# Optimization experiments

Hardware: AMD Instinct MI355X
Metric: run time of the kernel (lower is better)

The kernel has to match this reference:

```python
import jax, jax.numpy as jnp
import numpy as np

N = 4096       # voc_size
D = 256        # emb_dim
NEG = -9e15    # pyGAT mask value
ALPHA = 0.2    # LeakyReLU slope


def _row_normalize(a):
    rs = a.sum(axis=1, keepdims=True)
    inv = jnp.where(rs > 0, 1.0 / rs, 0.0)
    return a * inv


def setup_inputs() -> dict:
    key = jax.random.key(0)
    ks = jax.random.split(key, 10)
    # sparse-ish symmetric adjacency, then self-loops + row-normalize (GraphAT.normalize)
    raw = (jax.random.uniform(ks[0], (N, N)) < 0.01).astype(jnp.float32)
    raw = jnp.maximum(raw, raw.T)
    adj = _row_normalize(raw + jnp.eye(N, dtype=jnp.float32))
    x = jax.random.normal(ks[1], (N, N), dtype=jnp.float32) * 0.05
    def w(k, i, o):
        return jax.random.normal(k, (i, o), dtype=jnp.float32) * (1.0 / np.sqrt(i))
    return {
        "x": x, "adj": adj,
        "W11": w(ks[2], N, D), "a11": jax.random.normal(ks[3], (2 * D, 1), jnp.float32) * 0.1,
        "W12": w(ks[4], D, D), "a12": jax.random.normal(ks[5], (2 * D, 1), jnp.float32) * 0.1,
        "W21": w(ks[6], D, D), "a21": jax.random.normal(ks[7], (2 * D, 1), jnp.float32) * 0.1,
        "W22": w(ks[8], D, D), "a22": jax.random.normal(ks[9], (2 * D, 1), jnp.float32) * 0.1,
    }


def _gat_layer(h, adj, W, a):
    # Wh: [N, d_out]
    Wh = h @ W
    d_out = W.shape[1]
    f_src = Wh @ a[:d_out]          # [N, 1]
    f_dst = Wh @ a[d_out:]          # [N, 1]
    e = jax.nn.leaky_relu(f_src + f_dst.T, ALPHA)   # [N, N]
    e = jnp.where(adj > 0, e, NEG)
    attn = jax.nn.softmax(e, axis=1)
    return attn @ Wh                # [N, d_out]


def _gat(h, adj, Wa, aa, Wb, ab):
    # pyGAT GAT: multi-head (1 head) + ELU, then output attention layer + ELU
    h = jax.nn.elu(_gat_layer(h, adj, Wa, aa))
    return jax.nn.elu(_gat_layer(h, adj, Wb, ab))


def reference(x, adj, W11, a11, W12, a12, W21, a21, W22, a22):
    h = _gat(x, adj, W11, a11, W12, a12)
    h = jax.nn.relu(h)              # dropout(p=0.3) is identity in eval mode
    return _gat(h, adj, W21, a21, W22, a22)
```

## Files before the change

### kernel.cpp

```cpp
#include <hip/hip_runtime.h>
#include <hip/hip_bf16.h>
#include <cstdint>
#include <cstddef>

#define NV 4096
#define DE 256
#define MAXNNZ 192

typedef __attribute__((ext_vector_type(8))) short bf16x8;
typedef __attribute__((ext_vector_type(4))) float f32x4;

__device__ __forceinline__ unsigned short f2bf(float f) {
    unsigned int u = __float_as_uint(f);
    u += 0x7fff + ((u >> 16) & 1);
    return (unsigned short)(u >> 16);
}
__device__ __forceinline__ float bf2f(unsigned short h) {
    return __uint_as_float(((unsigned int)h) << 16);
}

__global__ __launch_bounds__(256) void build_csr(const float* __restrict__ adj,
                                                 int* __restrict__ cols,
                                                 int* __restrict__ nnz)
{
    int wave = threadIdx.x >> 6;
    int lane = threadIdx.x & 63;
    int row  = blockIdx.x * 4 + wave;
    const float* arow = adj + (size_t)row * NV;
    int* crow = cols + (size_t)row * MAXNNZ;
    int base = 0;
    for (int c0 = 0; c0 < NV; c0 += 64) {
        float v = arow[c0 + lane];
        bool pred = v > 0.0f;
        unsigned long long m = __ballot(pred);
        int idx = base + __popcll(m & ((1ull << lane) - 1ull));
        if (pred && idx < MAXNNZ) crow[idx] = c0 + lane;
        base += __popcll(m);
    }
    if (lane == 0) nnz[row] = base < MAXNNZ ? base : MAXNNZ;
}

__global__ __launch_bounds__(256) void transp_split(const float* __restrict__ W,
                                                    unsigned short* __restrict__ bh,
                                                    unsigned short* __restrict__ bl,
                                                    int K)
{
    __shared__ float tile[32][33];
    const int k0 = blockIdx.x * 32, n0 = blockIdx.y * 32;
    const int t = threadIdx.x;
    {
        int r = t >> 3, cq = t & 7;
        float4 v = *(const float4*)&W[(size_t)(k0 + r) * DE + n0 + cq * 4];
        tile[r][cq * 4 + 0] = v.x;
        tile[r][cq * 4 + 1] = v.y;
        tile[r][cq * 4 + 2] = v.z;
        tile[r][cq * 4 + 3] = v.w;
    }
    __syncthreads();
    {
        int nl = t >> 3, kq = t & 7;
        ushort4 hv, lv;
        float x0 = tile[kq * 4 + 0][nl];
        float x1 = tile[kq * 4 + 1][nl];
        float x2 = tile[kq * 4 + 2][nl];
        float x3 = tile[kq * 4 + 3][nl];
        hv.x = f2bf(x0); lv.x = f2bf(x0 - bf2f(hv.x));
        hv.y = f2bf(x1); lv.y = f2bf(x1 - bf2f(hv.y));
        hv.z = f2bf(x2); lv.z = f2bf(x2 - bf2f(hv.z));
        hv.w = f2bf(x3); lv.w = f2bf(x3 - bf2f(hv.w));
        size_t o = (size_t)(n0 + nl) * K + k0 + kq * 4;
        *(ushort4*)&bh[o] = hv;
        *(ushort4*)&bl[o] = lv;
    }
}

#define BM 64
#define BN 64
#define BK 32

__global__ __launch_bounds__(256) void gemm_split(const float* __restrict__ A,
                                                  const unsigned short* __restrict__ Bh,
                                                  const unsigned short* __restrict__ Bl,
                                                  float* __restrict__ C,
                                                  int K, int Kchunk)
{
    __shared__ __align__(16) unsigned short sA[64 * 64];
    __shared__ __align__(16) unsigned short sB[64 * 64];

    const int t    = threadIdx.x;
    const int lane = t & 63;
    const int wid  = t >> 6;
    const int wr   = wid >> 1;
    const int wc   = wid & 1;
    const int bn   = blockIdx.x * BN;
    const int bm   = blockIdx.y * BM;
    const int kz   = blockIdx.z;
    const int kbeg = kz * Kchunk;
    const int nsteps = Kchunk / BK;

    const int ar = t >> 2;
    const int as = t & 3;
    const int br = t >> 2;
    const int bq = t & 3;

    const float*          Ap  = A  + (size_t)(bm + ar) * K + kbeg + as * 8;
    const unsigned short* Bhp = Bh + (size_t)(bn + br) * K + kbeg + bq * 8;
    const unsigned short* Blp = Bl + (size_t)(bn + br) * K + kbeg + bq * 8;

    const int aw_h = ar * 64 + (((as)      ^ (ar & 7)) << 3);
    const int aw_l = ar * 64 + (((as | 4)  ^ (ar & 7)) << 3);
    const int bw_h = br * 64 + (((bq)      ^ (br & 7)) << 3);
    const int bw_l = br * 64 + (((bq | 4)  ^ (br & 7)) << 3);

    const int fr = lane & 15, fsub = lane >> 4;
    const int arow0 = wr * 32 + fr;
    const int arow1 = arow0 + 16;
    const int ard0h = arow0 * 64 + (((fsub)     ^ (arow0 & 7)) << 3);
    const int ard0l = arow0 * 64 + (((fsub | 4) ^ (arow0 & 7)) << 3);
    const int ard1h = arow1 * 64 + (((fsub)     ^ (arow1 & 7)) << 3);
    const int ard1l = arow1 * 64 + (((fsub | 4) ^ (arow1 & 7)) << 3);
    const int brow0 = wc * 32 + fr;
    const int brow1 = brow0 + 16;
    const int brd0h = brow0 * 64 + (((fsub)     ^ (brow0 & 7)) << 3);
    const int brd0l = brow0 * 64 + (((fsub | 4) ^ (brow0 & 7)) << 3);
    const int brd1h = brow1 * 64 + (((fsub)     ^ (brow1 & 7)) << 3);
    const int brd1l = brow1 * 64 + (((fsub | 4) ^ (brow1 & 7)) << 3);

    float4 a0 = *(const float4*)(Ap);
    float4 a1 = *(const float4*)(Ap + 4);
    bf16x8 g_bh = *(const bf16x8*)(Bhp);
    bf16x8 g_bl = *(const bf16x8*)(Blp);

    f32x4 acc[2][2];
#pragma unroll
    for (int i = 0; i < 2; ++i)
#pragma unroll
        for (int j = 0; j < 2; ++j) acc[i][j] = (f32x4){0.f, 0.f, 0.f, 0.f};

    for (int s = 0; s < nsteps; ++s) {
        __syncthreads();
        {
            float xs0 = a0.x, xs1 = a0.y, xs2 = a0.z, xs3 = a0.w;
            float xs4 = a1.x, xs5 = a1.y, xs6 = a1.z, xs7 = a1.w;
            bf16x8 hv, lv;
            unsigned short h;
            h = f2bf(xs0); hv[0] = (short)h; lv[0] = (short)f2bf(xs0 - bf2f(h));
            h = f2bf(xs1); hv[1] = (short)h; lv[1] = (short)f2bf(xs1 - bf2f(h));
            h = f2bf(xs2); hv[2] = (short)h; lv[2] = (short)f2bf(xs2 - bf2f(h));
            h = f2bf(xs3); hv[3] = (short)h; lv[3] = (short)f2bf(xs3 - bf2f(h));
            h = f2bf(xs4); hv[4] = (short)h; lv[4] = (short)f2bf(xs4 - bf2f(h));
            h = f2bf(xs5); hv[5] = (short)h; lv[5] = (short)f2bf(xs5 - bf2f(h));
            h = f2bf(xs6); hv[6] = (short)h; lv[6] = (short)f2bf(xs6 - bf2f(h));
            h = f2bf(xs7); hv[7] = (short)h; lv[7] = (short)f2bf(xs7 - bf2f(h));
            *(bf16x8*)&sA[aw_h] = hv;
            *(bf16x8*)&sA[aw_l] = lv;
        }
        *(bf16x8*)&sB[bw_h] = g_bh;
        *(bf16x8*)&sB[bw_l] = g_bl;
        __syncthreads();

        if (s + 1 < nsteps) {
            Ap += BK; Bhp += BK; Blp += BK;
            a0 = *(const float4*)(Ap);
            a1 = *(const float4*)(Ap + 4);
            g_bh = *(const bf16x8*)(Bhp);
            g_bl = *(const bf16x8*)(Blp);
        }

        bf16x8 ah0 = *(const bf16x8*)&sA[ard0h];
        bf16x8 al0 = *(const bf16x8*)&sA[ard0l];
        bf16x8 ah1 = *(const bf16x8*)&sA[ard1h];
        bf16x8 al1 = *(const bf16x8*)&sA[ard1l];
        bf16x8 bh0 = *(const bf16x8*)&sB[brd0h];
        bf16x8 bl0 = *(const bf16x8*)&sB[brd0l];
        bf16x8 bh1 = *(const bf16x8*)&sB[brd1h];
        bf16x8 bl1 = *(const bf16x8*)&sB[brd1l];

        acc[0][0] = __builtin_amdgcn_mfma_f32_16x16x32_bf16(ah0, bh0, acc[0][0], 0, 0, 0);
        acc[0][0] = __builtin_amdgcn_mfma_f32_16x16x32_bf16(ah0, bl0, acc[0][0], 0, 0, 0);
        acc[0][0] = __builtin_amdgcn_mfma_f32_16x16x32_bf16(al0, bh0, acc[0][0], 0, 0, 0);
        acc[0][1] = __builtin_amdgcn_mfma_f32_16x16x32_bf16(ah0, bh1, acc[0][1], 0, 0, 0);
        acc[0][1] = __builtin_amdgcn_mfma_f32_16x16x32_bf16(ah0, bl1, acc[0][1], 0, 0, 0);
        acc[0][1] = __builtin_amdgcn_mfma_f32_16x16x32_bf16(al0, bh1, acc[0][1], 0, 0, 0);
        acc[1][0] = __builtin_amdgcn_mfma_f32_16x16x32_bf16(ah1, bh0, acc[1][0], 0, 0, 0);
        acc[1][0] = __builtin_amdgcn_mfma_f32_16x16x32_bf16(ah1, bl0, acc[1][0], 0, 0, 0);
        acc[1][0] = __builtin_amdgcn_mfma_f32_16x16x32_bf16(al1, bh0, acc[1][0], 0, 0, 0);
        acc[1][1] = __builtin_amdgcn_mfma_f32_16x16x32_bf16(ah1, bh1, acc[1][1], 0, 0, 0);
        acc[1][1] = __builtin_amdgcn_mfma_f32_16x16x32_bf16(ah1, bl1, acc[1][1], 0, 0, 0);
        acc[1][1] = __builtin_amdgcn_mfma_f32_16x16x32_bf16(al1, bh1, acc[1][1], 0, 0, 0);
    }

    float* Cb = C + (size_t)kz * NV * DE;
#pragma unroll
    for (int mi = 0; mi < 2; ++mi) {
#pragma unroll
        for (int ni = 0; ni < 2; ++ni) {
            int row = bm + wr * 32 + mi * 16 + (fsub << 2);
            int col = bn + wc * 32 + ni * 16 + fr;
#pragma unroll
            for (int i = 0; i < 4; ++i)
                Cb[(size_t)(row + i) * DE + col] = acc[mi][ni][i];
        }
    }
}

__global__ __launch_bounds__(256) void reduce_fsd(const float* __restrict__ Cp,
                                                  const float* __restrict__ a,
                                                  float* __restrict__ Wh,
                                                  float* __restrict__ fs,
                                                  float* __restrict__ fd,
                                                  int S)
{
    int wid = threadIdx.x >> 6, lane = threadIdx.x & 63;
    int row = blockIdx.x * 4 + wid;
    size_t idx = (size_t)row * DE + lane * 4;
    float4 w = *(const float4*)&Cp[idx];
    for (int s = 1; s < S; ++s) {
        float4 p = *(const float4*)&Cp[(size_t)s * NV * DE + idx];
        w.x += p.x; w.y += p.y; w.z += p.z; w.w += p.w;
    }
    *(float4*)&Wh[idx] = w;
    float4 at = *(const float4*)&a[lane * 4];
    float4 ab = *(const float4*)&a[DE + lane * 4];
    float s = w.x * at.x + w.y * at.y + w.z * at.z + w.w * at.w;
    float d = w.x * ab.x + w.y * ab.y + w.z * ab.z + w.w * ab.w;
#pragma unroll
    for (int off = 32; off; off >>= 1) {
        s += __shfl_down(s, off);
        d += __shfl_down(d, off);
    }
    if (lane == 0) { fs[row] = s; fd[row] = d; }
}

template <int ACT>
__global__ __launch_bounds__(256) void attn_spmm(const float* __restrict__ Wh,
                                                 const float* __restrict__ fs,
                                                 const float* __restrict__ fd,
                                                 const int* __restrict__ cols,
                                                 const int* __restrict__ nnzArr,
                                                 float* __restrict__ out)
{
    __shared__ float p[MAXNNZ];
    __shared__ int   ci[MAXNNZ];
    __shared__ float red[4];
    __shared__ float part[4][DE];

    const int row = blockIdx.x;
    const int t   = threadIdx.x;
    const int lane = t & 63;
    const int wv   = t >> 6;
    const int n   = nnzArr[row];
    const int* rc = cols + (size_t)row * MAXNNZ;
    const float fsi = fs[row];

    float lm = -1e30f;
    for (int j = t; j < n; j += 256) {
        int c = rc[j];
        ci[j] = c;
        float e = fsi + fd[c];
        e = (e >= 0.0f) ? e : 0.2f * e;
        p[j] = e;
        lm = fmaxf(lm, e);
    }
#pragma unroll
    for (int off = 32; off; off >>= 1) lm = fmaxf(lm, __shfl_down(lm, off));
    if (lane == 0) red[wv] = lm;
    __syncthreads();
    const float m = fmaxf(fmaxf(red[0], red[1]), fmaxf(red[2], red[3]));
    __syncthreads();

    float ls = 0.0f;
    for (int j = t; j < n; j += 256) {
        float pe = expf(p[j] - m);
        p[j] = pe;
        ls += pe;
    }
#pragma unroll
    for (int off = 32; off; off >>= 1) ls += __shfl_down(ls, off);
    if (lane == 0) red[wv] = ls;
    __syncthreads();
    const float invZ = 1.0f / (red[0] + red[1] + red[2] + red[3]);

    const int d4 = lane * 4;
    f32x4 acc = (f32x4){0.f, 0.f, 0.f, 0.f};
    int j = wv;
    for (; j + 4 < n; j += 8) {
        float pj0 = p[j];     int c0 = ci[j];
        float pj1 = p[j + 4]; int c1 = ci[j + 4];
        float4 w0 = *(const float4*)&Wh[(size_t)c0 * DE + d4];
        float4 w1 = *(const float4*)&Wh[(size_t)c1 * DE + d4];
        acc.x = fmaf(pj0, w0.x, acc.x);
        acc.y = fmaf(pj0, w0.y, acc.y);
        acc.z = fmaf(pj0, w0.z, acc.z);
        acc.w = fmaf(pj0, w0.w, acc.w);
        acc.x = fmaf(pj1, w1.x, acc.x);
        acc.y = fmaf(pj1, w1.y, acc.y);
        acc.z = fmaf(pj1, w1.z, acc.z);
        acc.w = fmaf(pj1, w1.w, acc.w);
    }
    for (; j < n; j += 4) {
        float pj = p[j]; int c = ci[j];
        float4 w0 = *(const float4*)&Wh[(size_t)c * DE + d4];
        acc.x = fmaf(pj, w0.x, acc.x);
        acc.y = fmaf(pj, w0.y, acc.y);
        acc.z = fmaf(pj, w0.z, acc.z);
        acc.w = fmaf(pj, w0.w, acc.w);
    }
    *(f32x4*)&part[wv][d4] = acc;
    __syncthreads();

    float v = (part[0][t] + part[1][t]) + (part[2][t] + part[3][t]);
    v *= invZ;
    float r;
    if (ACT == 0) r = (v > 0.0f) ? v : expm1f(v);
    else          r = (v > 0.0f) ? v : 0.0f;
    out[(size_t)row * DE + t] = r;
}

extern "C" void kernel_launch(void* const* d_in, const int* in_sizes, int n_in,
                              void* d_out, int out_size, void* d_ws, size_t ws_size,
                              hipStream_t stream)
{
    const float* x   = (const float*)d_in[0];
    const float* adj = (const float*)d_in[1];
    const float* W11 = (const float*)d_in[2];
    const float* a11 = (const float*)d_in[3];
    const float* W12 = (const float*)d_in[4];
    const float* a12 = (const float*)d_in[5];
    const float* W21 = (const float*)d_in[6];
    const float* a21 = (const float*)d_in[7];
    const float* W22 = (const float*)d_in[8];
    const float* a22 = (const float*)d_in[9];
    float* out = (float*)d_out;

    char* ws = (char*)d_ws;
    size_t off = 0;
    int*   cols = (int*)(ws + off);            off += (size_t)NV * MAXNNZ * 4;
    int*   nnz  = (int*)(ws + off);            off += 16 * 1024;
    float* fs   = (float*)(ws + off);          off += 16 * 1024;
    float* fd   = (float*)(ws + off);          off += 16 * 1024;
    float* Wh   = (float*)(ws + off);          off += (size_t)NV * DE * 4;
    float* hA   = (float*)(ws + off);          off += (size_t)NV * DE * 4;
    unsigned short* BtH = (unsigned short*)(ws + off); off += (size_t)DE * NV * 2;
    unsigned short* BtL = (unsigned short*)(ws + off); off += (size_t)DE * NV * 2;
    float* Cpart = (float*)(ws + off);

    build_csr<<<NV / 4, 256, 0, stream>>>(adj, cols, nnz);

    transp_split<<<dim3(NV / 32, DE / 32), 256, 0, stream>>>(W11, BtH, BtL, NV);
    gemm_split<<<dim3(DE / BN, NV / BM, 4), 256, 0, stream>>>(x, BtH, BtL, Cpart, NV, NV / 4);
    reduce_fsd<<<NV / 4, 256, 0, stream>>>(Cpart, a11, Wh, fs, fd, 4);
    attn_spmm<0><<<NV, 256, 0, stream>>>(Wh, fs, fd, cols, nnz, hA);

    transp_split<<<dim3(DE / 32, DE / 32), 256, 0, stream>>>(W12, BtH, BtL, DE);
    gemm_split<<<dim3(DE / BN, NV / BM, 2), 256, 0, stream>>>(hA, BtH, BtL, Cpart, DE, DE / 2);
    reduce_fsd<<<NV / 4, 256, 0, stream>>>(Cpart, a12, Wh, fs, fd, 2);
    attn_spmm<1><<<NV, 256, 0, stream>>>(Wh, fs, fd, cols, nnz, hA);

    transp_split<<<dim3(DE / 32, DE / 32), 256, 0, stream>>>(W21, BtH, BtL, DE);
    gemm_split<<<dim3(DE / BN, NV / BM, 2), 256, 0, stream>>>(hA, BtH, BtL, Cpart, DE, DE / 2);
    reduce_fsd<<<NV / 4, 256, 0, stream>>>(Cpart, a21, Wh, fs, fd, 2);
    attn_spmm<0><<<NV, 256, 0, stream>>>(Wh, fs, fd, cols, nnz, hA);

    transp_split<<<dim3(DE / 32, DE / 32), 256, 0, stream>>>(W22, BtH, BtL, DE);
    gemm_split<<<dim3(DE / BN, NV / BM, 2), 256, 0, stream>>>(hA, BtH, BtL, Cpart, DE, DE / 2);
    reduce_fsd<<<NV / 4, 256, 0, stream>>>(Cpart, a22, Wh, fs, fd, 2);
    attn_spmm<0><<<NV, 256, 0, stream>>>(Wh, fs, fd, cols, nnz, out);
}
```

Measured before the change: 194.1 us.

## Enlarge GEMM tiles, add XCD-aware block remap, pre-split activations, vectorize CSR build

Replaces the 64x64 split-bf16 GEMM with a 128x128-tile version using a 4x4 MFMA accumulator grid per wave and an XCD-aware block index remap. The split-K factor is doubled. The attention SpMM kernel now writes its output pre-split into bf16 hi/lo arrays, so later GEMMs skip the per-tile fp32-to-bf16 split. The CSR builder reads the adjacency matrix with float4 loads. The larger tiles cut global re-reads of A and B, at the cost of more registers, fewer blocks and more split-K partials to reduce.

```diff
diff --git a/kernel.cpp b/kernel.cpp
--- a/kernel.cpp
+++ b/kernel.cpp
@@ -29,13 +29,17 @@
     const float* arow = adj + (size_t)row * NV;
     int* crow = cols + (size_t)row * MAXNNZ;
     int base = 0;
-    for (int c0 = 0; c0 < NV; c0 += 64) {
-        float v = arow[c0 + lane];
-        bool pred = v > 0.0f;
-        unsigned long long m = __ballot(pred);
-        int idx = base + __popcll(m & ((1ull << lane) - 1ull));
-        if (pred && idx < MAXNNZ) crow[idx] = c0 + lane;
-        base += __popcll(m);
+    for (int c0 = 0; c0 < NV; c0 += 256) {
+        float4 v = *(const float4*)&arow[c0 + lane * 4];
+        float vv[4] = {v.x, v.y, v.z, v.w};
+#pragma unroll
+        for (int e = 0; e < 4; ++e) {
+            bool pred = vv[e] > 0.0f;
+            unsigned long long m = __ballot(pred);
+            int idx = base + __popcll(m & ((1ull << lane) - 1ull));
+            if (pred && idx < MAXNNZ) crow[idx] = c0 + lane * 4 + e;
+            base += __popcll(m);
+        }
     }
     if (lane == 0) nnz[row] = base < MAXNNZ ? base : MAXNNZ;
 }
@@ -74,129 +78,139 @@
     }
 }
 
-#define BM 64
-#define BN 64
-#define BK 32
-
-__global__ __launch_bounds__(256) void gemm_split(const float* __restrict__ A,
+template <bool PRESPLIT>
+__global__ __launch_bounds__(256, 2) void gemm_bt(const float* __restrict__ Af,
+                                                  const unsigned short* __restrict__ Ah,
+                                                  const unsigned short* __restrict__ Al,
                                                   const unsigned short* __restrict__ Bh,
                                                   const unsigned short* __restrict__ Bl,
                                                   float* __restrict__ C,
                                                   int K, int Kchunk)
 {
-    __shared__ __align__(16) unsigned short sA[64 * 64];
-    __shared__ __align__(16) unsigned short sB[64 * 64];
-
-    const int t    = threadIdx.x;
-    const int lane = t & 63;
-    const int wid  = t >> 6;
-    const int wr   = wid >> 1;
-    const int wc   = wid & 1;
-    const int bn   = blockIdx.x * BN;
-    const int bm   = blockIdx.y * BM;
-    const int kz   = blockIdx.z;
+    __shared__ __align__(16) unsigned short sA[128 * 64];
+    __shared__ __align__(16) unsigned short sB[128 * 64];
+
+    const int t = threadIdx.x, lane = t & 63, wid = t >> 6;
+    const int wr = wid >> 1, wc = wid & 1;
+    const int KZ = K / Kchunk;
+
+    const int nwg = gridDim.x, orig = blockIdx.x;
+    const int q = nwg >> 3, r = nwg & 7;
+    const int xcd = orig & 7, jj = orig >> 3;
+    const int wgid = (xcd < r ? xcd * (q + 1) : r * (q + 1) + (xcd - r) * q) + jj;
+    const int row_t = wgid & 31;
+    const int kz    = (wgid >> 5) % KZ;
+    const int colt  = wgid / (32 * KZ);
+    const int bm = row_t * 128, bn = colt * 128;
     const int kbeg = kz * Kchunk;
-    const int nsteps = Kchunk / BK;
-
-    const int ar = t >> 2;
-    const int as = t & 3;
-    const int br = t >> 2;
-    const int bq = t & 3;
-
-    const float*          Ap  = A  + (size_t)(bm + ar) * K + kbeg + as * 8;
-    const unsigned short* Bhp = Bh + (size_t)(bn + br) * K + kbeg + bq * 8;
-    const unsigned short* Blp = Bl + (size_t)(bn + br) * K + kbeg + bq * 8;
-
-    const int aw_h = ar * 64 + (((as)      ^ (ar & 7)) << 3);
-    const int aw_l = ar * 64 + (((as | 4)  ^ (ar & 7)) << 3);
-    const int bw_h = br * 64 + (((bq)      ^ (br & 7)) << 3);
-    const int bw_l = br * 64 + (((bq | 4)  ^ (br & 7)) << 3);
+    const int nsteps = Kchunk / 32;
+
+    const int srow = t >> 1, shalf = t & 1;
+    const float*          Afp = Af ? (Af + (size_t)(bm + srow) * K + kbeg + shalf * 16) : nullptr;
+    const unsigned short* Ahp = Ah ? (Ah + (size_t)(bm + srow) * K + kbeg + shalf * 16) : nullptr;
+    const unsigned short* Alp = Al ? (Al + (size_t)(bm + srow) * K + kbeg + shalf * 16) : nullptr;
+    const unsigned short* Bhp = Bh + (size_t)(bn + srow) * K + kbeg + shalf * 16;
+    const unsigned short* Blp = Bl + (size_t)(bn + srow) * K + kbeg + shalf * 16;
+
+    const int c0 = shalf * 2;
+    const int wa0 = srow * 64 + (((c0)           ^ (srow & 7)) << 3);
+    const int wa1 = srow * 64 + (((c0 + 1)       ^ (srow & 7)) << 3);
+    const int wa2 = srow * 64 + (((c0 | 4)       ^ (srow & 7)) << 3);
+    const int wa3 = srow * 64 + ((((c0 + 1) | 4) ^ (srow & 7)) << 3);
 
     const int fr = lane & 15, fsub = lane >> 4;
-    const int arow0 = wr * 32 + fr;
-    const int arow1 = arow0 + 16;
-    const int ard0h = arow0 * 64 + (((fsub)     ^ (arow0 & 7)) << 3);
-    const int ard0l = arow0 * 64 + (((fsub | 4) ^ (arow0 & 7)) << 3);
-    const int ard1h = arow1 * 64 + (((fsub)     ^ (arow1 & 7)) << 3);
-    const int ard1l = arow1 * 64 + (((fsub | 4) ^ (arow1 & 7)) << 3);
-    const int brow0 = wc * 32 + fr;
-    const int brow1 = brow0 + 16;
-    const int brd0h = brow0 * 64 + (((fsub)     ^ (brow0 & 7)) << 3);
-    const int brd0l = brow0 * 64 + (((fsub | 4) ^ (brow0 & 7)) << 3);
-    const int brd1h = brow1 * 64 + (((fsub)     ^ (brow1 & 7)) << 3);
-    const int brd1l = brow1 * 64 + (((fsub | 4) ^ (brow1 & 7)) << 3);
-
-    float4 a0 = *(const float4*)(Ap);
-    float4 a1 = *(const float4*)(Ap + 4);
-    bf16x8 g_bh = *(const bf16x8*)(Bhp);
-    bf16x8 g_bl = *(const bf16x8*)(Blp);
-
-    f32x4 acc[2][2];
-#pragma unroll
-    for (int i = 0; i < 2; ++i)
-#pragma unroll
-        for (int j = 0; j < 2; ++j) acc[i][j] = (f32x4){0.f, 0.f, 0.f, 0.f};
+
+    bf16x8 gah0, gah1, gal0, gal1, gbh0, gbh1, gbl0, gbl1;
+
+#define LOAD_TILE()                                                          \
+    do {                                                                     \
+        if (PRESPLIT) {                                                      \
+            gah0 = *(const bf16x8*)(Ahp);                                    \
+            gah1 = *(const bf16x8*)(Ahp + 8);                                \
+            gal0 = *(const bf16x8*)(Alp);                                    \
+            gal1 = *(const bf16x8*)(Alp + 8);                                \
+        } else {                                                             \
+            float4 f0 = *(const float4*)(Afp);                               \
+            float4 f1 = *(const float4*)(Afp + 4);                           \
+            float4 f2 = *(const float4*)(Afp + 8);                           \
+            float4 f3 = *(const float4*)(Afp + 12);                          \
+            float xs[16] = {f0.x, f0.y, f0.z, f0.w, f1.x, f1.y, f1.z, f1.w,  \
+                            f2.x, f2.y, f2.z, f2.w, f3.x, f3.y, f3.z, f3.w}; \
+            _Pragma("unroll") for (int e = 0; e < 8; ++e) {                  \
+                unsigned short h = f2bf(xs[e]);                              \
+                gah0[e] = (short)h;                                          \
+                gal0[e] = (short)f2bf(xs[e] - bf2f(h));                      \
+            }                                                                \
+            _Pragma("unroll") for (int e = 0; e < 8; ++e) {                  \
+                unsigned short h = f2bf(xs[8 + e]);                          \
+                gah1[e] = (short)h;                                          \
+                gal1[e] = (short)f2bf(xs[8 + e] - bf2f(h));                  \
+            }                                                                \
+        }                                                                    \
+        gbh0 = *(const bf16x8*)(Bhp);                                        \
+        gbh1 = *(const bf16x8*)(Bhp + 8);                                    \
+        gbl0 = *(const bf16x8*)(Blp);                                        \
+        gbl1 = *(const bf16x8*)(Blp + 8);                                    \
+    } while (0)
+
+    LOAD_TILE();
+
+    f32x4 acc[4][4];
+#pragma unroll
+    for (int i = 0; i < 4; ++i)
+#pragma unroll
+        for (int j2 = 0; j2 < 4; ++j2) acc[i][j2] = (f32x4){0.f, 0.f, 0.f, 0.f};
 
     for (int s = 0; s < nsteps; ++s) {
         __syncthreads();
-        {
-            float xs0 = a0.x, xs1 = a0.y, xs2 = a0.z, xs3 = a0.w;
-            float xs4 = a1.x, xs5 = a1.y, xs6 = a1.z, xs7 = a1.w;
-            bf16x8 hv, lv;
-            unsigned short h;
-            h = f2bf(xs0); hv[0] = (short)h; lv[0] = (short)f2bf(xs0 - bf2f(h));
-            h = f2bf(xs1); hv[1] = (short)h; lv[1] = (short)f2bf(xs1 - bf2f(h));
-            h = f2bf(xs2); hv[2] = (short)h; lv[2] = (short)f2bf(xs2 - bf2f(h));
-            h = f2bf(xs3); hv[3] = (short)h; lv[3] = (short)f2bf(xs3 - bf2f(h));
-            h = f2bf(xs4); hv[4] = (short)h; lv[4] = (short)f2bf(xs4 - bf2f(h));
-            h = f2bf(xs5); hv[5] = (short)h; lv[5] = (short)f2bf(xs5 - bf2f(h));
-            h = f2bf(xs6); hv[6] = (short)h; lv[6] = (short)f2bf(xs6 - bf2f(h));
-            h = f2bf(xs7); hv[7] = (short)h; lv[7] = (short)f2bf(xs7 - bf2f(h));
-            *(bf16x8*)&sA[aw_h] = hv;
-            *(bf16x8*)&sA[aw_l] = lv;
-        }
-        *(bf16x8*)&sB[bw_h] = g_bh;
-        *(bf16x8*)&sB[bw_l] = g_bl;
+        *(bf16x8*)&sA[wa0] = gah0;
+        *(bf16x8*)&sA[wa1] = gah1;
+        *(bf16x8*)&sA[wa2] = gal0;
+        *(bf16x8*)&sA[wa3] = gal1;
+        *(bf16x8*)&sB[wa0] = gbh0;
+        *(bf16x8*)&sB[wa1] = gbh1;
+        *(bf16x8*)&sB[wa2] = gbl0;
+        *(bf16x8*)&sB[wa3] = gbl1;
         __syncthreads();
 
         if (s + 1 < nsteps) {
-            Ap += BK; Bhp += BK; Blp += BK;
-            a0 = *(const float4*)(Ap);
-            a1 = *(const float4*)(Ap + 4);
-            g_bh = *(const bf16x8*)(Bhp);
-            g_bl = *(const bf16x8*)(Blp);
-        }
-
-        bf16x8 ah0 = *(const bf16x8*)&sA[ard0h];
-        bf16x8 al0 = *(const bf16x8*)&sA[ard0l];
-        bf16x8 ah1 = *(const bf16x8*)&sA[ard1h];
-        bf16x8 al1 = *(const bf16x8*)&sA[ard1l];
-        bf16x8 bh0 = *(const bf16x8*)&sB[brd0h];
-        bf16x8 bl0 = *(const bf16x8*)&sB[brd0l];
-        bf16x8 bh1 = *(const bf16x8*)&sB[brd1h];
-        bf16x8 bl1 = *(const bf16x8*)&sB[brd1l];
-
-        acc[0][0] = __builtin_amdgcn_mfma_f32_16x16x32_bf16(ah0, bh0, acc[0][0], 0, 0, 0);
-        acc[0][0] = __builtin_amdgcn_mfma_f32_16x16x32_bf16(ah0, bl0, acc[0][0], 0, 0, 0);
-        acc[0][0] = __builtin_amdgcn_mfma_f32_16x16x32_bf16(al0, bh0, acc[0][0], 0, 0, 0);
-        acc[0][1] = __builtin_amdgcn_mfma_f32_16x16x32_bf16(ah0, bh1, acc[0][1], 0, 0, 0);
-        acc[0][1] = __builtin_amdgcn_mfma_f32_16x16x32_bf16(ah0, bl1, acc[0][1], 0, 0, 0);
-        acc[0][1] = __builtin_amdgcn_mfma_f32_16x16x32_bf16(al0, bh1, acc[0][1], 0, 0, 0);
-        acc[1][0] = __builtin_amdgcn_mfma_f32_16x16x32_bf16(ah1, bh0, acc[1][0], 0, 0, 0);
-        acc[1][0] = __builtin_amdgcn_mfma_f32_16x16x32_bf16(ah1, bl0, acc[1][0], 0, 0, 0);
-        acc[1][0] = __builtin_amdgcn_mfma_f32_16x16x32_bf16(al1, bh0, acc[1][0], 0, 0, 0);
-        acc[1][1] = __builtin_amdgcn_mfma_f32_16x16x32_bf16(ah1, bh1, acc[1][1], 0, 0, 0);
-        acc[1][1] = __builtin_amdgcn_mfma_f32_16x16x32_bf16(ah1, bl1, acc[1][1], 0, 0, 0);
-        acc[1][1] = __builtin_amdgcn_mfma_f32_16x16x32_bf16(al1, bh1, acc[1][1], 0, 0, 0);
-    }
+            if (PRESPLIT) { Ahp += 32; Alp += 32; }
+            else          { Afp += 32; }
+            Bhp += 32; Blp += 32;
+            LOAD_TILE();
+        }
+
+        bf16x8 fah[4], fal[4], fbh[4], fbl[4];
+#pragma unroll
+        for (int mi = 0; mi < 4; ++mi) {
+            int row = wr * 64 + mi * 16 + fr;
+            fah[mi] = *(const bf16x8*)&sA[row * 64 + (((fsub)     ^ (row & 7)) << 3)];
+            fal[mi] = *(const bf16x8*)&sA[row * 64 + (((fsub | 4) ^ (row & 7)) << 3)];
+        }
+#pragma unroll
+        for (int ni = 0; ni < 4; ++ni) {
+            int row = wc * 64 + ni * 16 + fr;
+            fbh[ni] = *(const bf16x8*)&sB[row * 64 + (((fsub)     ^ (row & 7)) << 3)];
+            fbl[ni] = *(const bf16x8*)&sB[row * 64 + (((fsub | 4) ^ (row & 7)) << 3)];
+        }
+#pragma unroll
+        for (int mi = 0; mi < 4; ++mi)
+#pragma unroll
+            for (int ni = 0; ni < 4; ++ni) {
+                acc[mi][ni] = __builtin_amdgcn_mfma_f32_16x16x32_bf16(fah[mi], fbh[ni], acc[mi][ni], 0, 0, 0);
+                acc[mi][ni] = __builtin_amdgcn_mfma_f32_16x16x32_bf16(fah[mi], fbl[ni], acc[mi][ni], 0, 0, 0);
+                acc[mi][ni] = __builtin_amdgcn_mfma_f32_16x16x32_bf16(fal[mi], fbh[ni], acc[mi][ni], 0, 0, 0);
+            }
+    }
+#undef LOAD_TILE
 
     float* Cb = C + (size_t)kz * NV * DE;
 #pragma unroll
-    for (int mi = 0; mi < 2; ++mi) {
-#pragma unroll
-        for (int ni = 0; ni < 2; ++ni) {
-            int row = bm + wr * 32 + mi * 16 + (fsub << 2);
-            int col = bn + wc * 32 + ni * 16 + fr;
+    for (int mi = 0; mi < 4; ++mi) {
+#pragma unroll
+        for (int ni = 0; ni < 4; ++ni) {
+            int row = bm + wr * 64 + mi * 16 + (fsub << 2);
+            int col = bn + wc * 64 + ni * 16 + fr;
 #pragma unroll
             for (int i = 0; i < 4; ++i)
                 Cb[(size_t)(row + i) * DE + col] = acc[mi][ni][i];
@@ -232,13 +246,15 @@
     if (lane == 0) { fs[row] = s; fd[row] = d; }
 }
 
-template <int ACT>
+template <int ACT, bool SPLIT>
 __global__ __launch_bounds__(256) void attn_spmm(const float* __restrict__ Wh,
                                                  const float* __restrict__ fs,
                                                  const float* __restrict__ fd,
                                                  const int* __restrict__ cols,
                                                  const int* __restrict__ nnzArr,
-                                                 float* __restrict__ out)
+                                                 float* __restrict__ out,
+                                                 unsigned short* __restrict__ hh,
+                                                 unsigned short* __restrict__ hl)
 {
     __shared__ float p[MAXNNZ];
     __shared__ int   ci[MAXNNZ];
@@ -311,10 +327,17 @@
 
     float v = (part[0][t] + part[1][t]) + (part[2][t] + part[3][t]);
     v *= invZ;
-    float r;
-    if (ACT == 0) r = (v > 0.0f) ? v : expm1f(v);
-    else          r = (v > 0.0f) ? v : 0.0f;
-    out[(size_t)row * DE + t] = r;
+    float rres;
+    if (ACT == 0) rres = (v > 0.0f) ? v : expm1f(v);
+    else          rres = (v > 0.0f) ? v : 0.0f;
+
+    if (SPLIT) {
+        unsigned short h = f2bf(rres);
+        hh[(size_t)row * DE + t] = h;
+        hl[(size_t)row * DE + t] = f2bf(rres - bf2f(h));
+    } else {
+        out[(size_t)row * DE + t] = rres;
+    }
 }
 
 extern "C" void kernel_launch(void* const* d_in, const int* in_sizes, int n_in,
@@ -340,7 +363,8 @@
     float* fs   = (float*)(ws + off);          off += 16 * 1024;
     float* fd   = (float*)(ws + off);          off += 16 * 1024;
     float* Wh   = (float*)(ws + off);          off += (size_t)NV * DE * 4;
-    float* hA   = (float*)(ws + off);          off += (size_t)NV * DE * 4;
+    unsigned short* hh  = (unsigned short*)(ws + off); off += (size_t)NV * DE * 2;
+    unsigned short* hl  = (unsigned short*)(ws + off); off += (size_t)NV * DE * 2;
     unsigned short* BtH = (unsigned short*)(ws + off); off += (size_t)DE * NV * 2;
     unsigned short* BtL = (unsigned short*)(ws + off); off += (size_t)DE * NV * 2;
     float* Cpart = (float*)(ws + off);
@@ -348,22 +372,26 @@
     build_csr<<<NV / 4, 256, 0, stream>>>(adj, cols, nnz);
 
     transp_split<<<dim3(NV / 32, DE / 32), 256, 0, stream>>>(W11, BtH, BtL, NV);
-    gemm_split<<<dim3(DE / BN, NV / BM, 4), 256, 0, stream>>>(x, BtH, BtL, Cpart, NV, NV / 4);
-    reduce_fsd<<<NV / 4, 256, 0, stream>>>(Cpart, a11, Wh, fs, fd, 4);
-    attn_spmm<0><<<NV, 256, 0, stream>>>(Wh, fs, fd, cols, nnz, hA);
+    gemm_bt<false><<<2 * 8 * 32, 256, 0, stream>>>(x, nullptr, nullptr, BtH, BtL,
+                                                   Cpart, NV, NV / 8);
+    reduce_fsd<<<NV / 4, 256, 0, stream>>>(Cpart, a11, Wh, fs, fd, 8);
+    attn_spmm<0, true><<<NV, 256, 0, stream>>>(Wh, fs, fd, cols, nnz, nullptr, hh, hl);
 
     transp_split<<<dim3(DE / 32, DE / 32), 256, 0, stream>>>(W12, BtH, BtL, DE);
-    gemm_split<<<dim3(DE / BN, NV / BM, 2), 256, 0, stream>>>(hA, BtH, BtL, Cpart, DE, DE / 2);
-    reduce_fsd<<<NV / 4, 256, 0, stream>>>(Cpart, a12, Wh, fs, fd, 2);
-    attn_spmm<1><<<NV, 256, 0, stream>>>(Wh, fs, fd, cols, nnz, hA);
+    gemm_bt<true><<<2 * 4 * 32, 256, 0, stream>>>(nullptr, hh, hl, BtH, BtL,
+                                                  Cpart, DE, DE / 4);
+    reduce_fsd<<<NV / 4, 256, 0, stream>>>(Cpart, a12, Wh, fs, fd, 4);
+    attn_spmm<1, true><<<NV, 256, 0, stream>>>(Wh, fs, fd, cols, nnz, nullptr, hh, hl);
 
     transp_split<<<dim3(DE / 32, DE / 32), 256, 0, stream>>>(W21, BtH, BtL, DE);
-    gemm_split<<<dim3(DE / BN, NV / BM, 2), 256, 0, stream>>>(hA, BtH, BtL, Cpart, DE, DE / 2);
-    reduce_fsd<<<NV / 4, 256, 0, stream>>>(Cpart, a21, Wh, fs, fd, 2);
-    attn_spmm<0><<<NV, 256, 0, stream>>>(Wh, fs, fd, cols, nnz, hA);
+    gemm_bt<true><<<2 * 4 * 32, 256, 0, stream>>>(nullptr, hh, hl, BtH, BtL,
+                                                  Cpart, DE, DE / 4);
+    reduce_fsd<<<NV / 4, 256, 0, stream>>>(Cpart, a21, Wh, fs, fd, 4);
+    attn_spmm<0, true><<<NV, 256, 0, stream>>>(Wh, fs, fd, cols, nnz, nullptr, hh, hl);
 
     transp_split<<<dim3(DE / 32, DE / 32), 256, 0, stream>>>(W22, BtH, BtL, DE);
-    gemm_split<<<dim3(DE / BN, NV / BM, 2), 256, 0, stream>>>(hA, BtH, BtL, Cpart, DE, DE / 2);
-    reduce_fsd<<<NV / 4, 256, 0, stream>>>(Cpart, a22, Wh, fs, fd, 2);
-    attn_spmm<0><<<NV, 256, 0, stream>>>(Wh, fs, fd, cols, nnz, out);
-}
+    gemm_bt<true><<<2 * 4 * 32, 256, 0, stream>>>(nullptr, hh, hl, BtH, BtL,
+                                                  Cpart, DE, DE / 4);
+    reduce_fsd<<<NV / 4, 256, 0, stream>>>(Cpart, a22, Wh, fs, fd, 4);
+    attn_spmm<0, false><<<NV, 256, 0, stream>>>(Wh, fs, fd, cols, nnz, out, nullptr, nullptr);
+}
```

Result: faster. 184.5 us (-4.9%).
